# Optimization experiments

Measured on AMD Instinct MI355X. Metric: run time of the kernel, lower is better.

The kernel has to match this reference:

```python
import jax, jax.numpy as jnp
from jax import lax
import numpy as np

B = 33  # block size hard-coded in the original model
BB = B * B  # 1089


def _blockify(img):
    # img: [S, H*33, L*33] -> [1089, L*H*S], column order (l major, h, s)
    S = img.shape[0]; H = img.shape[1] // B; L = img.shape[2] // B
    x = img.reshape(S, H, B, L, B).transpose(3, 1, 0, 2, 4)  # [L,H,S,33,33]
    return x.reshape(L * H * S, BB).T


def _unblockify(X, S, H, L):
    # X: [1089, L*H*S] -> [S, H*33, L*33]
    x = X.T.reshape(L, H, S, B, B).transpose(2, 1, 3, 0, 4)  # [S,H,33,L,33]
    return x.reshape(S, H * B, L * B)


def _conv(x, w):
    return lax.conv_general_dilated(x, w, (1, 1), 'SAME',
                                    dimension_numbers=('NCHW', 'OIHW', 'NCHW'))


def _cnn(x, w1, b1, w2, b2, w3, b3, w4):
    # 4-layer CNN used by both Denoiser and Deblocker; x: [N,1,h,w]
    x = jax.nn.relu(_conv(x, w1) + b1[None, :, None, None])
    x = jax.nn.relu(_conv(x, w2) + b2[None, :, None, None])
    x = jax.nn.relu(_conv(x, w3) + b3[None, :, None, None])
    return _conv(x, w4)  # final conv has no bias


def _denoise(X, w1, b1, w2, b2, w3, b3, w4):
    # X: [1089, N] -> per-block CNN -> [1089, N]
    N = X.shape[1]
    x = X.T.reshape(N, 1, B, B)
    out = _cnn(x, w1, b1, w2, b2, w3, b3, w4)
    return out[:, 0].reshape(N, BB).T


def _deblock(img, w1, b1, w2, b2, w3, b3, w4):
    # img: [S, Hp, Wp] -> [S, Hp, Wp]
    return _cnn(img[:, None], w1, b1, w2, b2, w3, b3, w4)[:, 0]


def setup_inputs() -> dict:
    key = jax.random.key(0)
    ks = jax.random.split(key, 20)
    S, H, L, M, layers = 8, 8, 8, 272, 5
    wstd = 0.05
    def w(k, shape):
        return jax.random.normal(k, shape, jnp.float32) * wstd
    inp = {}
    inp['inputs'] = jax.random.normal(ks[0], (S, 1, H * B, L * B), jnp.float32)
    A = jax.random.normal(ks[1], (M, BB), jnp.float32) / np.float32(np.sqrt(BB))
    inp['A'] = A
    inp['Q'] = A.T
    inp['steps'] = jnp.ones((layers,), jnp.float32)
    inp['den_w1'] = w(ks[2], (layers, 32, 1, 3, 3))
    inp['den_b1'] = jnp.zeros((layers, 32), jnp.float32)
    inp['den_w2'] = w(ks[3], (layers, 32, 32, 3, 3))
    inp['den_b2'] = jnp.zeros((layers, 32), jnp.float32)
    inp['den_w3'] = w(ks[4], (layers, 32, 32, 3, 3))
    inp['den_b3'] = jnp.zeros((layers, 32), jnp.float32)
    inp['den_w4'] = w(ks[5], (layers, 1, 32, 3, 3))
    inp['deb_w1'] = w(ks[6], (layers, 32, 1, 3, 3))
    inp['deb_b1'] = jnp.zeros((layers, 32), jnp.float32)
    inp['deb_w2'] = w(ks[7], (layers, 32, 32, 3, 3))
    inp['deb_b2'] = jnp.zeros((layers, 32), jnp.float32)
    inp['deb_w3'] = w(ks[8], (layers, 32, 32, 3, 3))
    inp['deb_b3'] = jnp.zeros((layers, 32), jnp.float32)
    inp['deb_w4'] = w(ks[9], (layers, 1, 32, 3, 3))
    inp['output_layers'] = layers
    return inp


def reference(inputs, A, Q, steps,
              den_w1, den_b1, den_w2, den_b2, den_w3, den_b3, den_w4,
              deb_w1, deb_b1, deb_w2, deb_b2, deb_w3, deb_b3, deb_w4,
              output_layers):
    S = inputs.shape[0]
    H = inputs.shape[2] // B
    L = inputs.shape[3] // B
    Xb = _blockify(inputs[:, 0])          # [1089, N]
    y = A @ Xb                             # sampling: [M, N]
    X = Q @ y                              # initial reconstruction [1089, N]
    I = jnp.eye(BB, dtype=A.dtype)
    AtA = A.T @ A                          # original recomputes each layer; same math
    for n in range(output_layers):
        step = steps[n]
        z = step * (A.T @ (y - A @ X)) + X
        noise = _denoise(X, den_w1[n], den_b1[n], den_w2[n], den_b2[n],
                         den_w3[n], den_b3[n], den_w4[n])
        X = z - (step * AtA - I) @ noise
        img = _unblockify(X, S, H, L)
        img = img - _deblock(img, deb_w1[n], deb_b1[n], deb_w2[n], deb_b2[n],
                             deb_w3[n], deb_b3[n], deb_w4[n])
        X = _blockify(img)
    return _unblockify(X, S, H, L)[:, None]  # [S,1,H*33,L*33]
```

## Files before the change

### kernel.cpp

```cpp
#include <hip/hip_runtime.h>
#include <hip/hip_fp16.h>

#define BLKSZ 33
#define NBB   1089
#define IMW   264

typedef _Float16 f16x8 __attribute__((ext_vector_type(8)));
typedef float f32x4 __attribute__((ext_vector_type(4)));

__global__ __launch_bounds__(256) void blockify_k(const float* __restrict__ in,
                                                  float* __restrict__ X, int S) {
  int gid = blockIdx.x * 256 + threadIdx.x;
  int total = S * 64 * NBB;
  if (gid >= total) return;
  int n = gid / NBB, p = gid - n * NBB;
  int l = n >> 6, h = (n >> 3) & 7, s = n & 7;
  int i = p / BLKSZ, j = p - i * BLKSZ;
  X[gid] = in[((size_t)s * IMW + h * BLKSZ + i) * IMW + l * BLKSZ + j];
}

__global__ __launch_bounds__(256) void gemm_nt_sk(
    const float* __restrict__ Am, const float* __restrict__ Bm,
    float* __restrict__ P, int M, int N, int K, int lda, int ldb, int SK) {
  __shared__ float As[16][68];
  __shared__ float Bs[16][68];
  int tid = threadIdx.x;
  int tx = tid & 15, ty = tid >> 4;
  int bi = blockIdx.y * 64, bj = blockIdx.x * 64;
  int sk = blockIdx.z;
  int chunk = (((K + SK - 1) / SK) + 15) & ~15;
  int kbeg = sk * chunk;
  int kend = kbeg + chunk; if (kend > K) kend = K;
  float acc[4][4] = {{0.f, 0.f, 0.f, 0.f}, {0.f, 0.f, 0.f, 0.f},
                     {0.f, 0.f, 0.f, 0.f}, {0.f, 0.f, 0.f, 0.f}};
  float ra[4], rb[4];
  {
    int kk = kbeg + tx;
#pragma unroll
    for (int t = 0; t < 4; ++t) {
      int r = ty + t * 16;
      ra[t] = (bi + r < M && kk < kend) ? Am[(size_t)(bi + r) * lda + kk] : 0.f;
      rb[t] = (bj + r < N && kk < kend) ? Bm[(size_t)(bj + r) * ldb + kk] : 0.f;
    }
  }
  for (int k0 = kbeg; k0 < kend; k0 += 16) {
#pragma unroll
    for (int t = 0; t < 4; ++t) {
      int r = ty + t * 16;
      As[tx][r] = ra[t];
      Bs[tx][r] = rb[t];
    }
    __syncthreads();
    if (k0 + 16 < kend) {
      int kk = k0 + 16 + tx;
#pragma unroll
      for (int t = 0; t < 4; ++t) {
        int r = ty + t * 16;
        ra[t] = (bi + r < M && kk < kend) ? Am[(size_t)(bi + r) * lda + kk] : 0.f;
        rb[t] = (bj + r < N && kk < kend) ? Bm[(size_t)(bj + r) * ldb + kk] : 0.f;
      }
    }
#pragma unroll
    for (int kk = 0; kk < 16; ++kk) {
      float4 av = *(const float4*)&As[kk][ty * 4];
      float4 bv = *(const float4*)&Bs[kk][tx * 4];
      acc[0][0] += av.x * bv.x; acc[0][1] += av.x * bv.y; acc[0][2] += av.x * bv.z; acc[0][3] += av.x * bv.w;
      acc[1][0] += av.y * bv.x; acc[1][1] += av.y * bv.y; acc[1][2] += av.y * bv.z; acc[1][3] += av.y * bv.w;
      acc[2][0] += av.z * bv.x; acc[2][1] += av.z * bv.y; acc[2][2] += av.z * bv.z; acc[2][3] += av.z * bv.w;
      acc[3][0] += av.w * bv.x; acc[3][1] += av.w * bv.y; acc[3][2] += av.w * bv.z; acc[3][3] += av.w * bv.w;
    }
    __syncthreads();
  }
  size_t base = (size_t)sk * M * N;
#pragma unroll
  for (int r = 0; r < 4; ++r) {
    int i = bi + ty * 4 + r;
    if (i >= M) continue;
#pragma unroll
    for (int c = 0; c < 4; ++c) {
      int j = bj + tx * 4 + c;
      if (j < N) P[base + (size_t)i * N + j] = acc[r][c];
    }
  }
}

__global__ __launch_bounds__(256) void reduce_sk_k(
    const float* __restrict__ P, float* __restrict__ C, float* __restrict__ C2,
    long long total, long long stride, int SK, int mode,
    const float* __restrict__ step_ptr, const float* __restrict__ src1,
    const float* __restrict__ src2) {
  long long gid = (long long)blockIdx.x * 256 + threadIdx.x;
  if (gid >= total) return;
  float s = 0.f;
  for (int k = 0; k < SK; ++k) s += P[(size_t)k * stride + gid];
  if (mode == 0) {
    C[gid] = s;
    if (C2) C2[gid] = s;
  } else {
    float st = step_ptr[0];
    float v = src1[gid] - st * s + st * src2[gid];
    int n = (int)(gid / NBB), p = (int)(gid - (long long)n * NBB);
    int l = n >> 6, h = (n >> 3) & 7, s_ = n & 7;
    int i = p / BLKSZ, j = p - i * BLKSZ;
    C[((size_t)s_ * IMW + h * BLKSZ + i) * IMW + l * BLKSZ + j] = v;
  }
}

__global__ __launch_bounds__(256) void pack_w_k(const float* __restrict__ w0,
                                                const float* __restrict__ w1,
                                                const float* __restrict__ w2,
                                                const float* __restrict__ w3,
                                                __half* __restrict__ wp, int layers) {
  int gid = blockIdx.x * 256 + threadIdx.x;
  int total = layers * 4 * 9216;
  if (gid >= total) return;
  int slot = gid / 9216, r = gid - slot * 9216;
  int n = slot >> 2, which = slot & 3;
  int tap = r / 1024, r2 = r - tap * 1024;
  int co = r2 >> 5, ci = r2 & 31;
  const float* src = (which == 0) ? w0 : (which == 1) ? w1 : (which == 2) ? w2 : w3;
  wp[gid] = __float2half(src[n * 9216 + (co * 32 + ci) * 9 + tap]);
}

__global__ __launch_bounds__(256) void zero_borders1_k(__half* __restrict__ a,
                                                       int nimg, int H, int W) {
  int Wp = W + 2, Hp = H + 2;
  int perim = 2 * Wp + 2 * H;
  int gid = blockIdx.x * 256 + threadIdx.x;
  int total = nimg * perim;
  if (gid >= total) return;
  int img = gid / perim, k = gid - img * perim;
  int row, col;
  if (k < Wp)            { row = 0;      col = k; }
  else if (k < 2 * Wp)   { row = Hp - 1; col = k - Wp; }
  else { int k2 = k - 2 * Wp; row = 1 + (k2 >> 1); col = (k2 & 1) ? (Wp - 1) : 0; }
  size_t off = ((size_t)(img * Hp + row) * Wp + col) * 32;
  float4 z = {0.f, 0.f, 0.f, 0.f};
  float4* pa = (float4*)(a + off);
#pragma unroll
  for (int q = 0; q < 4; ++q) pa[q] = z;
}

__global__ __launch_bounds__(256) void conv1_k(const float* __restrict__ in,
                                               __half* __restrict__ out,
                                               const float* __restrict__ w,
                                               const float* __restrict__ b,
                                               int nimg, int H, int W) {
  __shared__ float wl[9][32];
  __shared__ float bl[32];
  int tid = threadIdx.x;
  for (int t = tid; t < 288; t += 256) {
    int co = t / 9, tap = t - co * 9;
    wl[tap][co] = w[t];
  }
  if (tid < 32) bl[tid] = b[tid];
  __syncthreads();
  int Hp = H + 2, Wp = W + 2;
  int gid = blockIdx.x * 256 + tid;
  if (gid >= nimg * Hp * Wp) return;
  int img = gid / (Hp * Wp);
  int rem = gid - img * (Hp * Wp);
  int yy = rem / Wp, xx = rem - yy * Wp;
  size_t ob = ((size_t)(img * Hp + yy) * Wp + xx) * 32;
  if (yy == 0 || yy == Hp - 1 || xx == 0 || xx == Wp - 1) {
    float4 z = {0.f, 0.f, 0.f, 0.f};
#pragma unroll
    for (int q = 0; q < 4; ++q) *(float4*)(out + ob + 8 * q) = z;
    return;
  }
  int y = yy - 1, x = xx - 1;
  float acc[32];
#pragma unroll
  for (int c = 0; c < 32; ++c) acc[c] = bl[c];
  const float* ip = in + (size_t)img * H * W;
#pragma unroll
  for (int ty = 0; ty < 3; ++ty)
#pragma unroll
    for (int tx = 0; tx < 3; ++tx) {
      int yv = y + ty - 1, xv = x + tx - 1;
      if (yv >= 0 && yv < H && xv >= 0 && xv < W) {
        float v = ip[(size_t)yv * W + xv];
        const float* wp = &wl[ty * 3 + tx][0];
#pragma unroll
        for (int q = 0; q < 8; ++q) {
          float4 wv = *(const float4*)(wp + q * 4);
          acc[q * 4 + 0] += v * wv.x; acc[q * 4 + 1] += v * wv.y;
          acc[q * 4 + 2] += v * wv.z; acc[q * 4 + 3] += v * wv.w;
        }
      }
    }
  __half2* op = (__half2*)(out + ob);
#pragma unroll
  for (int c2 = 0; c2 < 16; ++c2)
    op[c2] = __floats2half2_rn(fmaxf(acc[2 * c2], 0.f), fmaxf(acc[2 * c2 + 1], 0.f));
}

__global__ __launch_bounds__(256) void conv2_mfma_k(const __half* __restrict__ in,
                                                    __half* __restrict__ out,
                                                    const __half* __restrict__ wp,
                                                    const float* __restrict__ bias,
                                                    int nimg, int H, int W, int CH) {
  int ntx = (W + 15) >> 4;
  int nch = (H + CH - 1) / CH;
  int wid = blockIdx.x * 4 + (threadIdx.x >> 6);
  int total = nimg * 2 * ntx * nch;
  if (wid >= total) return;
  int lane = threadIdx.x & 63;
  int m16 = lane & 15, kg = lane >> 4;
  int yc = wid % nch; int t = wid / nch;
  int xt = t % ntx; t /= ntx;
  int cohalf = t & 1; int img = t >> 1;
  int Wp = W + 2, Hp = H + 2, Hpm1 = Hp - 1;
  const __half* wq = wp + (cohalf * 16 + m16) * 32 + kg * 8;
  f16x8 bfr0 = *(const f16x8*)(wq + 0 * 1024);
  f16x8 bfr1 = *(const f16x8*)(wq + 1 * 1024);
  f16x8 bfr2 = *(const f16x8*)(wq + 2 * 1024);
  f16x8 bfr3 = *(const f16x8*)(wq + 3 * 1024);
  f16x8 bfr4 = *(const f16x8*)(wq + 4 * 1024);
  f16x8 bfr5 = *(const f16x8*)(wq + 5 * 1024);
  f16x8 bfr6 = *(const f16x8*)(wq + 6 * 1024);
  f16x8 bfr7 = *(const f16x8*)(wq + 7 * 1024);
  f16x8 bfr8 = *(const f16x8*)(wq + 8 * 1024);
  float bv = bias[cohalf * 16 + m16];
  int x0 = xt << 4;
  int y1 = yc * CH + 1;
  int y2 = y1 + CH - 1; if (y2 > H) y2 = H;
  int c0 = x0 + m16;     if (c0 > W + 1) c0 = W + 1; c0 *= 32;
  int c1 = x0 + m16 + 1; if (c1 > W + 1) c1 = W + 1; c1 *= 32;
  int c2 = x0 + m16 + 2; if (c2 > W + 1) c2 = W + 1; c2 *= 32;
  size_t ibase = (size_t)img * Hp;
  int cohalf16 = cohalf * 16;

#define LOADROW(row, d0, d1, d2) { int rr = (row); if (rr > Hpm1) rr = Hpm1;    \
    const __half* rp = in + (ibase + rr) * (size_t)Wp * 32 + kg * 8;            \
    d0 = *(const f16x8*)(rp + c0); d1 = *(const f16x8*)(rp + c1);               \
    d2 = *(const f16x8*)(rp + c2); }

#define CITER(yo, A0_,A1_,A2_, B0_,B1_,B2_, C0_,C1_,C2_, P0_,P1_,P2_) {         \
    LOADROW((yo) + 3, P0_, P1_, P2_);                                           \
    f32x4 a0 = {0.f, 0.f, 0.f, 0.f}, a1 = {0.f, 0.f, 0.f, 0.f};                 \
    a0 = __builtin_amdgcn_mfma_f32_16x16x32_f16(A0_, bfr0, a0, 0, 0, 0);        \
    a1 = __builtin_amdgcn_mfma_f32_16x16x32_f16(A1_, bfr1, a1, 0, 0, 0);        \
    a0 = __builtin_amdgcn_mfma_f32_16x16x32_f16(A2_, bfr2, a0, 0, 0, 0);        \
    a1 = __builtin_amdgcn_mfma_f32_16x16x32_f16(B0_, bfr3, a1, 0, 0, 0);        \
    a0 = __builtin_amdgcn_mfma_f32_16x16x32_f16(B1_, bfr4, a0, 0, 0, 0);        \
    a1 = __builtin_amdgcn_mfma_f32_16x16x32_f16(B2_, bfr5, a1, 0, 0, 0);        \
    a0 = __builtin_amdgcn_mfma_f32_16x16x32_f16(C0_, bfr6, a0, 0, 0, 0);        \
    a1 = __builtin_amdgcn_mfma_f32_16x16x32_f16(C1_, bfr7, a1, 0, 0, 0);        \
    a0 = __builtin_amdgcn_mfma_f32_16x16x32_f16(C2_, bfr8, a0, 0, 0, 0);        \
    __half* op = out + (ibase + (yo)) * (size_t)Wp * 32 + cohalf16 + m16;       \
    _Pragma("unroll")                                                           \
    for (int r = 0; r < 4; ++r) { int xo = x0 + kg * 4 + r;                     \
      if (xo < W) op[(xo + 1) * 32] = __float2half(fmaxf(a0[r] + a1[r] + bv, 0.f)); } }

  f16x8 A0,A1,A2,B0,B1,B2,C0,C1,C2,D0,D1,D2,E0,E1,E2;
  LOADROW(y1 - 1, A0, A1, A2);
  LOADROW(y1,     B0, B1, B2);
  LOADROW(y1 + 1, C0, C1, C2);
  LOADROW(y1 + 2, D0, D1, D2);
  int yo = y1;
  for (; yo + 4 <= y2; yo += 5) {
    CITER(yo,     A0,A1,A2, B0,B1,B2, C0,C1,C2, E0,E1,E2);
    CITER(yo + 1, B0,B1,B2, C0,C1,C2, D0,D1,D2, A0,A1,A2);
    CITER(yo + 2, C0,C1,C2, D0,D1,D2, E0,E1,E2, B0,B1,B2);
    CITER(yo + 3, D0,D1,D2, E0,E1,E2, A0,A1,A2, C0,C1,C2);
    CITER(yo + 4, E0,E1,E2, A0,A1,A2, B0,B1,B2, D0,D1,D2);
  }
  if (yo <= y2) { CITER(yo, A0,A1,A2, B0,B1,B2, C0,C1,C2, E0,E1,E2); ++yo; }
  if (yo <= y2) { CITER(yo, B0,B1,B2, C0,C1,C2, D0,D1,D2, A0,A1,A2); ++yo; }
  if (yo <= y2) { CITER(yo, C0,C1,C2, D0,D1,D2, E0,E1,E2, B0,B1,B2); ++yo; }
  if (yo <= y2) { CITER(yo, D0,D1,D2, E0,E1,E2, A0,A1,A2, C0,C1,C2); ++yo; }
#undef CITER
#undef LOADROW
}

__global__ __launch_bounds__(256) void conv4_k(const __half* __restrict__ in,
                                               float* __restrict__ out,
                                               const float* __restrict__ w,
                                               const float* __restrict__ src,
                                               int nimg, int H, int W, float sign, int perm) {
  __shared__ float wl[9][32];
  int tid = threadIdx.x;
  for (int t = tid; t < 288; t += 256) {
    int ci = t / 9, tap = t - ci * 9;
    wl[tap][ci] = w[t];
  }
  __syncthreads();
  int gid = blockIdx.x * 256 + tid;
  if (gid >= nimg * H * W) return;
  int img = gid / (H * W);
  int rem = gid - img * H * W;
  int y = rem / W, x = rem - y * W;
  int Wp = W + 2;
  float acc = 0.f;
#pragma unroll
  for (int ty = 0; ty < 3; ++ty)
#pragma unroll
    for (int tx = 0; tx < 3; ++tx) {
      const f16x8* ip = (const f16x8*)(in + ((size_t)(img * (H + 2) + y + ty) * Wp + x + tx) * 32);
      const float* wpt = &wl[ty * 3 + tx][0];
#pragma unroll
      for (int q = 0; q < 4; ++q) {
        f16x8 v = ip[q];
#pragma unroll
        for (int e = 0; e < 8; ++e) acc += (float)v[e] * wpt[q * 8 + e];
      }
    }
  float val = src[gid] + sign * acc;
  if (perm) {
    int h = y / BLKSZ, i = y - h * BLKSZ;
    int l = x / BLKSZ, j = x - l * BLKSZ;
    out[(size_t)(l * 64 + h * 8 + img) * NBB + i * BLKSZ + j] = val;
  } else {
    out[gid] = val;
  }
}

__global__ __launch_bounds__(256) void denoise_fused_k(
    const float* __restrict__ X, float* __restrict__ T,
    const float* __restrict__ w1, const float* __restrict__ b1,
    const __half* __restrict__ wp2, const float* __restrict__ b2,
    const __half* __restrict__ wp3, const float* __restrict__ b3,
    const float* __restrict__ w4) {
  __shared__ __align__(16) __half Abuf[35 * 35 * 32];
  __shared__ __align__(16) __half Bbuf[35 * 35 * 32];
  __shared__ float wl1[9][32];
  __shared__ float wl4[9][32];
  __shared__ float bl1[32];
  int tid = threadIdx.x;
  int img = blockIdx.x;
  int wave = tid >> 6, lane = tid & 63;
  int m16 = lane & 15, kg = lane >> 4;

  for (int t = tid; t < 288; t += 256) {
    int c = t / 9, tap = t - c * 9;
    wl1[tap][c] = w1[t];
    wl4[tap][c] = w4[t];
  }
  if (tid < 32) bl1[tid] = b1[tid];
  float* Xs = (float*)Bbuf;
  const float* Xg = X + (size_t)img * NBB;
  for (int t = tid; t < NBB; t += 256) Xs[t] = Xg[t];
  __syncthreads();

  for (int cell = tid; cell < 1225; cell += 256) {
    int yy = cell / 35, xx = cell - yy * 35;
    __half* oc = Abuf + cell * 32;
    if (yy == 0 || yy == 34 || xx == 0 || xx == 34) {
      f16x8 hz = {};
#pragma unroll
      for (int q = 0; q < 4; ++q) *(f16x8*)(oc + 8 * q) = hz;
      continue;
    }
    int y = yy - 1, x = xx - 1;
    float acc[32];
#pragma unroll
    for (int c = 0; c < 32; ++c) acc[c] = bl1[c];
#pragma unroll
    for (int dy = 0; dy < 3; ++dy)
#pragma unroll
      for (int dx = 0; dx < 3; ++dx) {
        int yv = y + dy - 1, xv = x + dx - 1;
        if (yv >= 0 && yv < 33 && xv >= 0 && xv < 33) {
          float v = Xs[yv * 33 + xv];
          const float* wp = &wl1[dy * 3 + dx][0];
#pragma unroll
          for (int q = 0; q < 8; ++q) {
            float4 wv = *(const float4*)(wp + q * 4);
            acc[q * 4 + 0] += v * wv.x; acc[q * 4 + 1] += v * wv.y;
            acc[q * 4 + 2] += v * wv.z; acc[q * 4 + 3] += v * wv.w;
          }
        }
      }
    __half2* op = (__half2*)oc;
#pragma unroll
    for (int c2 = 0; c2 < 16; ++c2)
      op[c2] = __floats2half2_rn(fmaxf(acc[2 * c2], 0.f), fmaxf(acc[2 * c2 + 1], 0.f));
  }
  __syncthreads();

#define CONV2LDS(SRC, DST, WPTR, BPTR) {                                        \
  _Pragma("unroll 1")                                                           \
  for (int jid = wave; jid < 12; jid += 4) {                                    \
    int cohalf = jid & 1;                                                       \
    int xt = (jid >> 1) % 3;                                                    \
    int yh = jid / 6;                                                           \
    const __half* wq = WPTR + (cohalf * 16 + m16) * 32 + kg * 8;                \
    f16x8 bfr0 = *(const f16x8*)(wq + 0 * 1024);                                \
    f16x8 bfr1 = *(const f16x8*)(wq + 1 * 1024);                                \
    f16x8 bfr2 = *(const f16x8*)(wq + 2 * 1024);                                \
    f16x8 bfr3 = *(const f16x8*)(wq + 3 * 1024);                                \
    f16x8 bfr4 = *(const f16x8*)(wq + 4 * 1024);                                \
    f16x8 bfr5 = *(const f16x8*)(wq + 5 * 1024);                                \
    f16x8 bfr6 = *(const f16x8*)(wq + 6 * 1024);                                \
    f16x8 bfr7 = *(const f16x8*)(wq + 7 * 1024);                                \
    f16x8 bfr8 = *(const f16x8*)(wq + 8 * 1024);                                \
    float bv = BPTR[cohalf * 16 + m16];                                         \
    int x0 = xt << 4;                                                           \
    int y1 = 1 + yh * 17;                                                       \
    int y2 = yh ? 33 : 17;                                                      \
    int c0 = x0 + m16;     if (c0 > 34) c0 = 34; c0 *= 32;                      \
    int c1 = x0 + m16 + 1; if (c1 > 34) c1 = 34; c1 *= 32;                      \
    int c2 = x0 + m16 + 2; if (c2 > 34) c2 = 34; c2 *= 32;                      \
    int cohalf16 = cohalf * 16;                                                 \
    f16x8 A0,A1,A2,B0,B1,B2,C0,C1,C2,D0,D1,D2,E0,E1,E2;                         \
    LROW(SRC, y1 - 1, A0, A1, A2);                                              \
    LROW(SRC, y1,     B0, B1, B2);                                              \
    LROW(SRC, y1 + 1, C0, C1, C2);                                              \
    LROW(SRC, y1 + 2, D0, D1, D2);                                              \
    int yo = y1;                                                                \
    for (; yo + 4 <= y2; yo += 5) {                                             \
      CIT(SRC, DST, yo,     A0,A1,A2, B0,B1,B2, C0,C1,C2, E0,E1,E2);            \
      CIT(SRC, DST, yo + 1, B0,B1,B2, C0,C1,C2, D0,D1,D2, A0,A1,A2);            \
      CIT(SRC, DST, yo + 2, C0,C1,C2, D0,D1,D2, E0,E1,E2, B0,B1,B2);            \
      CIT(SRC, DST, yo + 3, D0,D1,D2, E0,E1,E2, A0,A1,A2, C0,C1,C2);            \
      CIT(SRC, DST, yo + 4, E0,E1,E2, A0,A1,A2, B0,B1,B2, D0,D1,D2);            \
    }                                                                           \
    if (yo <= y2) { CIT(SRC, DST, yo, A0,A1,A2, B0,B1,B2, C0,C1,C2, E0,E1,E2); ++yo; } \
    if (yo <= y2) { CIT(SRC, DST, yo, B0,B1,B2, C0,C1,C2, D0,D1,D2, A0,A1,A2); ++yo; } \
    if (yo <= y2) { CIT(SRC, DST, yo, C0,C1,C2, D0,D1,D2, E0,E1,E2, B0,B1,B2); ++yo; } \
    if (yo <= y2) { CIT(SRC, DST, yo, D0,D1,D2, E0,E1,E2, A0,A1,A2, C0,C1,C2); ++yo; } \
  } }

#define LROW(SRC, row, d0, d1, d2) { int rr = (row); if (rr > 34) rr = 34;      \
    const __half* rp = SRC + rr * 35 * 32 + kg * 8;                             \
    d0 = *(const f16x8*)(rp + c0); d1 = *(const f16x8*)(rp + c1);               \
    d2 = *(const f16x8*)(rp + c2); }

#define CIT(SRC, DST, yo, A0_,A1_,A2_, B0_,B1_,B2_, C0_,C1_,C2_, P0_,P1_,P2_) { \
    LROW(SRC, (yo) + 3, P0_, P1_, P2_);                                         \
    f32x4 a0 = {0.f, 0.f, 0.f, 0.f}, a1 = {0.f, 0.f, 0.f, 0.f};                 \
    a0 = __builtin_amdgcn_mfma_f32_16x16x32_f16(A0_, bfr0, a0, 0, 0, 0);        \
    a1 = __builtin_amdgcn_mfma_f32_16x16x32_f16(A1_, bfr1, a1, 0, 0, 0);        \
    a0 = __builtin_amdgcn_mfma_f32_16x16x32_f16(A2_, bfr2, a0, 0, 0, 0);        \
    a1 = __builtin_amdgcn_mfma_f32_16x16x32_f16(B0_, bfr3, a1, 0, 0, 0);        \
    a0 = __builtin_amdgcn_mfma_f32_16x16x32_f16(B1_, bfr4, a0, 0, 0, 0);        \
    a1 = __builtin_amdgcn_mfma_f32_16x16x32_f16(B2_, bfr5, a1, 0, 0, 0);        \
    a0 = __builtin_amdgcn_mfma_f32_16x16x32_f16(C0_, bfr6, a0, 0, 0, 0);        \
    a1 = __builtin_amdgcn_mfma_f32_16x16x32_f16(C1_, bfr7, a1, 0, 0, 0);        \
    a0 = __builtin_amdgcn_mfma_f32_16x16x32_f16(C2_, bfr8, a0, 0, 0, 0);        \
    _Pragma("unroll")                                                           \
    for (int r = 0; r < 4; ++r) { int xo = x0 + kg * 4 + r;                     \
      if (xo < 33) DST[(yo) * 35 * 32 + (xo + 1) * 32 + cohalf16 + m16] =       \
        __float2half(fmaxf(a0[r] + a1[r] + bv, 0.f)); } }

  {
    f16x8 hz = {};
    for (int t = tid; t < 544; t += 256) {
      int ci = t >> 2, q = t & 3;
      int cell;
      if (ci < 35)       cell = ci;
      else if (ci < 70)  cell = 34 * 35 + (ci - 35);
      else if (ci < 103) cell = (ci - 70 + 1) * 35;
      else               cell = (ci - 103 + 1) * 35 + 34;
      *(f16x8*)(Bbuf + cell * 32 + q * 8) = hz;
    }
  }
  CONV2LDS(Abuf, Bbuf, wp2, b2);
  __syncthreads();

  CONV2LDS(Bbuf, Abuf, wp3, b3);
  __syncthreads();
#undef CIT
#undef LROW
#undef CONV2LDS

  float* Tg = T + (size_t)img * NBB;
  for (int p = tid; p < NBB; p += 256) {
    int y = p / 33, x = p - y * 33;
    float acc = 0.f;
#pragma unroll
    for (int dy = 0; dy < 3; ++dy)
#pragma unroll
      for (int dx = 0; dx < 3; ++dx) {
        const f16x8* ip = (const f16x8*)(Abuf + ((y + dy) * 35 + x + dx) * 32);
        const float* wpt = &wl4[dy * 3 + dx][0];
#pragma unroll
        for (int q = 0; q < 4; ++q) {
          f16x8 v = ip[q];
#pragma unroll
          for (int e = 0; e < 8; ++e) acc += (float)v[e] * wpt[q * 8 + e];
        }
      }
    Tg[p] = Xg[p] + acc;
  }
}

static inline int cdiv(int a, int b) { return (a + b - 1) / b; }

extern "C" void kernel_launch(void* const* d_in, const int* in_sizes, int n_in,
                              void* d_out, int out_size, void* d_ws, size_t ws_size,
                              hipStream_t stream) {
  const float* d_inputs = (const float*)d_in[0];
  const float* d_A      = (const float*)d_in[1];
  const float* d_Q      = (const float*)d_in[2];
  const float* d_steps  = (const float*)d_in[3];
  const float* den_w1 = (const float*)d_in[4];
  const float* den_b1 = (const float*)d_in[5];
  const float* den_b2 = (const float*)d_in[7];
  const float* den_b3 = (const float*)d_in[9];
  const float* den_w4 = (const float*)d_in[10];
  const float* deb_w1 = (const float*)d_in[11];
  const float* deb_b1 = (const float*)d_in[12];
  const float* deb_b2 = (const float*)d_in[14];
  const float* deb_b3 = (const float*)d_in[16];
  const float* deb_w4 = (const float*)d_in[17];

  int layers = in_sizes[3];
  int M      = in_sizes[1] / NBB;
  int S      = in_sizes[0] / (IMW * IMW);
  int N      = 64 * S;

  float* ws    = (float*)d_ws;
  float* AtA   = ws;
  float* X     = AtA + 1185936;
  float* T     = X + (size_t)N * NBB;
  float* X0    = T + (size_t)N * NBB;
  float* y2    = X0 + (size_t)N * NBB;
  float* img   = y2 + (size_t)N * M;
  float* Pbuf  = img + (size_t)S * IMW * IMW;
  __half* wph  = (__half*)(Pbuf + (size_t)8 * N * NBB);
  __half* buf1 = wph + (size_t)layers * 4 * 9216 + 2048;
  size_t bufElems = (size_t)S * 266 * 266 * 32;
  __half* buf2 = buf1 + bufElems;

  dim3 blk(256);

  pack_w_k<<<cdiv(layers * 4 * 9216, 256), blk, 0, stream>>>(
      (const float*)d_in[6], (const float*)d_in[8], (const float*)d_in[13],
      (const float*)d_in[15], wph, layers);
  blockify_k<<<cdiv(N * NBB, 256), blk, 0, stream>>>(d_inputs, T, S);

  gemm_nt_sk<<<dim3(cdiv(NBB, 64), cdiv(NBB, 64), 2), blk, 0, stream>>>(
      d_Q, d_Q, Pbuf, NBB, NBB, M, M, M, 2);
  reduce_sk_k<<<cdiv(NBB * NBB, 256), blk, 0, stream>>>(
      Pbuf, AtA, nullptr, (long long)NBB * NBB, (long long)NBB * NBB, 2, 0,
      nullptr, nullptr, nullptr);
  gemm_nt_sk<<<dim3(cdiv(M, 64), cdiv(N, 64), 8), blk, 0, stream>>>(
      T, d_A, Pbuf, N, M, NBB, NBB, NBB, 8);
  reduce_sk_k<<<cdiv(N * M, 256), blk, 0, stream>>>(
      Pbuf, y2, nullptr, (long long)N * M, (long long)N * M, 8, 0,
      nullptr, nullptr, nullptr);
  gemm_nt_sk<<<dim3(cdiv(NBB, 64), cdiv(N, 64), 4), blk, 0, stream>>>(
      y2, d_Q, Pbuf, N, NBB, M, M, M, 4);
  reduce_sk_k<<<cdiv(N * NBB, 256), blk, 0, stream>>>(
      Pbuf, X0, X, (long long)N * NBB, (long long)N * NBB, 4, 0,
      nullptr, nullptr, nullptr);

  const int CH_DEB = 12;
  int deb_waves = S * 2 * cdiv(IMW, 16) * cdiv(IMW, CH_DEB);

  for (int n = 0; n < layers; ++n) {
    const float* stepp = d_steps + n;

    denoise_fused_k<<<N, blk, 0, stream>>>(
        X, T, den_w1 + n * 288, den_b1 + n * 32,
        wph + (size_t)(n * 4 + 0) * 9216, den_b2 + n * 32,
        wph + (size_t)(n * 4 + 1) * 9216, den_b3 + n * 32,
        den_w4 + n * 288);

    gemm_nt_sk<<<dim3(cdiv(NBB, 64), cdiv(N, 64), 8), blk, 0, stream>>>(
        T, AtA, Pbuf, N, NBB, NBB, NBB, NBB, 8);
    reduce_sk_k<<<cdiv(N * NBB, 256), blk, 0, stream>>>(
        Pbuf, img, nullptr, (long long)N * NBB, (long long)N * NBB, 8, 4,
        stepp, T, X0);

    zero_borders1_k<<<cdiv(S * (2 * 266 + 2 * 264), 256), blk, 0, stream>>>(
        buf2, S, IMW, IMW);
    conv1_k<<<cdiv(S * 266 * 266, 256), blk, 0, stream>>>(
        img, buf1, deb_w1 + n * 288, deb_b1 + n * 32, S, IMW, IMW);
    conv2_mfma_k<<<cdiv(deb_waves, 4), blk, 0, stream>>>(
        buf1, buf2, wph + (size_t)(n * 4 + 2) * 9216, deb_b2 + n * 32, S, IMW, IMW, CH_DEB);
    conv2_mfma_k<<<cdiv(deb_waves, 4), blk, 0, stream>>>(
        buf2, buf1, wph + (size_t)(n * 4 + 3) * 9216, deb_b3 + n * 32, S, IMW, IMW, CH_DEB);
    if (n < layers - 1) {
      conv4_k<<<cdiv(S * IMW * IMW, 256), blk, 0, stream>>>(
          buf1, X, deb_w4 + n * 288, img, S, IMW, IMW, -1.f, 1);
    } else {
      conv4_k<<<cdiv(S * IMW * IMW, 256), blk, 0, stream>>>(
          buf1, (float*)d_out, deb_w4 + n * 288, img, S, IMW, IMW, -1.f, 0);
    }
  }
}
```

Baseline: 1.288 ms.

## Compute both output-channel halves per wave, use fdot2 in final conv, widen denoiser block

In the deblocker's MFMA conv, each wave now produces all 32 output channels, so every loaded input row feeds both channel halves and input loads are halved, at the cost of holding twice the weight fragments in registers. The final 32-to-1 convolutions (conv4_k and the denoiser tail) keep their weights as packed fp16 pairs and use the fdot2 builtin instead of scalar fp32 multiply-adds, which adds fp16 rounding of the weights. The fused denoiser kernel moves from 256 to 512 threads, splits the conv work into 24 smaller row jobs, and adds a barrier after border zeroing.

```diff
diff --git a/kernel.cpp b/kernel.cpp
--- a/kernel.cpp
+++ b/kernel.cpp
@@ -6,7 +6,16 @@
 #define IMW   264
 
 typedef _Float16 f16x8 __attribute__((ext_vector_type(8)));
+typedef _Float16 f16x2 __attribute__((ext_vector_type(2)));
 typedef float f32x4 __attribute__((ext_vector_type(4)));
+
+__device__ __forceinline__ float dot2f(f16x2 a, f16x2 b, float c) {
+#if __has_builtin(__builtin_amdgcn_fdot2)
+  return __builtin_amdgcn_fdot2(a, b, c, false);
+#else
+  return c + (float)a[0] * (float)b[0] + (float)a[1] * (float)b[1];
+#endif
+}
 
 __global__ __launch_bounds__(256) void blockify_k(const float* __restrict__ in,
                                                   float* __restrict__ X, int S) {
@@ -203,25 +212,25 @@
   int ntx = (W + 15) >> 4;
   int nch = (H + CH - 1) / CH;
   int wid = blockIdx.x * 4 + (threadIdx.x >> 6);
-  int total = nimg * 2 * ntx * nch;
+  int total = nimg * ntx * nch;
   if (wid >= total) return;
   int lane = threadIdx.x & 63;
   int m16 = lane & 15, kg = lane >> 4;
   int yc = wid % nch; int t = wid / nch;
-  int xt = t % ntx; t /= ntx;
-  int cohalf = t & 1; int img = t >> 1;
+  int xt = t % ntx; int img = t / ntx;
   int Wp = W + 2, Hp = H + 2, Hpm1 = Hp - 1;
-  const __half* wq = wp + (cohalf * 16 + m16) * 32 + kg * 8;
-  f16x8 bfr0 = *(const f16x8*)(wq + 0 * 1024);
-  f16x8 bfr1 = *(const f16x8*)(wq + 1 * 1024);
-  f16x8 bfr2 = *(const f16x8*)(wq + 2 * 1024);
-  f16x8 bfr3 = *(const f16x8*)(wq + 3 * 1024);
-  f16x8 bfr4 = *(const f16x8*)(wq + 4 * 1024);
-  f16x8 bfr5 = *(const f16x8*)(wq + 5 * 1024);
-  f16x8 bfr6 = *(const f16x8*)(wq + 6 * 1024);
-  f16x8 bfr7 = *(const f16x8*)(wq + 7 * 1024);
-  f16x8 bfr8 = *(const f16x8*)(wq + 8 * 1024);
-  float bv = bias[cohalf * 16 + m16];
+  const __half* wqA = wp + m16 * 32 + kg * 8;
+  const __half* wqB = wp + (16 + m16) * 32 + kg * 8;
+  f16x8 bA0 = *(const f16x8*)(wqA + 0 * 1024), bB0 = *(const f16x8*)(wqB + 0 * 1024);
+  f16x8 bA1 = *(const f16x8*)(wqA + 1 * 1024), bB1 = *(const f16x8*)(wqB + 1 * 1024);
+  f16x8 bA2 = *(const f16x8*)(wqA + 2 * 1024), bB2 = *(const f16x8*)(wqB + 2 * 1024);
+  f16x8 bA3 = *(const f16x8*)(wqA + 3 * 1024), bB3 = *(const f16x8*)(wqB + 3 * 1024);
+  f16x8 bA4 = *(const f16x8*)(wqA + 4 * 1024), bB4 = *(const f16x8*)(wqB + 4 * 1024);
+  f16x8 bA5 = *(const f16x8*)(wqA + 5 * 1024), bB5 = *(const f16x8*)(wqB + 5 * 1024);
+  f16x8 bA6 = *(const f16x8*)(wqA + 6 * 1024), bB6 = *(const f16x8*)(wqB + 6 * 1024);
+  f16x8 bA7 = *(const f16x8*)(wqA + 7 * 1024), bB7 = *(const f16x8*)(wqB + 7 * 1024);
+  f16x8 bA8 = *(const f16x8*)(wqA + 8 * 1024), bB8 = *(const f16x8*)(wqB + 8 * 1024);
+  float bvA = bias[m16], bvB = bias[16 + m16];
   int x0 = xt << 4;
   int y1 = yc * CH + 1;
   int y2 = y1 + CH - 1; if (y2 > H) y2 = H;
@@ -229,7 +238,6 @@
   int c1 = x0 + m16 + 1; if (c1 > W + 1) c1 = W + 1; c1 *= 32;
   int c2 = x0 + m16 + 2; if (c2 > W + 1) c2 = W + 1; c2 *= 32;
   size_t ibase = (size_t)img * Hp;
-  int cohalf16 = cohalf * 16;
 
 #define LOADROW(row, d0, d1, d2) { int rr = (row); if (rr > Hpm1) rr = Hpm1;    \
     const __half* rp = in + (ibase + rr) * (size_t)Wp * 32 + kg * 8;            \
@@ -238,20 +246,32 @@
 
 #define CITER(yo, A0_,A1_,A2_, B0_,B1_,B2_, C0_,C1_,C2_, P0_,P1_,P2_) {         \
     LOADROW((yo) + 3, P0_, P1_, P2_);                                           \
-    f32x4 a0 = {0.f, 0.f, 0.f, 0.f}, a1 = {0.f, 0.f, 0.f, 0.f};                 \
-    a0 = __builtin_amdgcn_mfma_f32_16x16x32_f16(A0_, bfr0, a0, 0, 0, 0);        \
-    a1 = __builtin_amdgcn_mfma_f32_16x16x32_f16(A1_, bfr1, a1, 0, 0, 0);        \
-    a0 = __builtin_amdgcn_mfma_f32_16x16x32_f16(A2_, bfr2, a0, 0, 0, 0);        \
-    a1 = __builtin_amdgcn_mfma_f32_16x16x32_f16(B0_, bfr3, a1, 0, 0, 0);        \
-    a0 = __builtin_amdgcn_mfma_f32_16x16x32_f16(B1_, bfr4, a0, 0, 0, 0);        \
-    a1 = __builtin_amdgcn_mfma_f32_16x16x32_f16(B2_, bfr5, a1, 0, 0, 0);        \
-    a0 = __builtin_amdgcn_mfma_f32_16x16x32_f16(C0_, bfr6, a0, 0, 0, 0);        \
-    a1 = __builtin_amdgcn_mfma_f32_16x16x32_f16(C1_, bfr7, a1, 0, 0, 0);        \
-    a0 = __builtin_amdgcn_mfma_f32_16x16x32_f16(C2_, bfr8, a0, 0, 0, 0);        \
-    __half* op = out + (ibase + (yo)) * (size_t)Wp * 32 + cohalf16 + m16;       \
+    f32x4 aA0 = {0.f,0.f,0.f,0.f}, aA1 = {0.f,0.f,0.f,0.f};                     \
+    f32x4 aB0 = {0.f,0.f,0.f,0.f}, aB1 = {0.f,0.f,0.f,0.f};                     \
+    aA0 = __builtin_amdgcn_mfma_f32_16x16x32_f16(A0_, bA0, aA0, 0, 0, 0);       \
+    aB0 = __builtin_amdgcn_mfma_f32_16x16x32_f16(A0_, bB0, aB0, 0, 0, 0);       \
+    aA1 = __builtin_amdgcn_mfma_f32_16x16x32_f16(A1_, bA1, aA1, 0, 0, 0);       \
+    aB1 = __builtin_amdgcn_mfma_f32_16x16x32_f16(A1_, bB1, aB1, 0, 0, 0);       \
+    aA0 = __builtin_amdgcn_mfma_f32_16x16x32_f16(A2_, bA2, aA0, 0, 0, 0);       \
+    aB0 = __builtin_amdgcn_mfma_f32_16x16x32_f16(A2_, bB2, aB0, 0, 0, 0);       \
+    aA1 = __builtin_amdgcn_mfma_f32_16x16x32_f16(B0_, bA3, aA1, 0, 0, 0);       \
+    aB1 = __builtin_amdgcn_mfma_f32_16x16x32_f16(B0_, bB3, aB1, 0, 0, 0);       \
+    aA0 = __builtin_amdgcn_mfma_f32_16x16x32_f16(B1_, bA4, aA0, 0, 0, 0);       \
+    aB0 = __builtin_amdgcn_mfma_f32_16x16x32_f16(B1_, bB4, aB0, 0, 0, 0);       \
+    aA1 = __builtin_amdgcn_mfma_f32_16x16x32_f16(B2_, bA5, aA1, 0, 0, 0);       \
+    aB1 = __builtin_amdgcn_mfma_f32_16x16x32_f16(B2_, bB5, aB1, 0, 0, 0);       \
+    aA0 = __builtin_amdgcn_mfma_f32_16x16x32_f16(C0_, bA6, aA0, 0, 0, 0);       \
+    aB0 = __builtin_amdgcn_mfma_f32_16x16x32_f16(C0_, bB6, aB0, 0, 0, 0);       \
+    aA1 = __builtin_amdgcn_mfma_f32_16x16x32_f16(C1_, bA7, aA1, 0, 0, 0);       \
+    aB1 = __builtin_amdgcn_mfma_f32_16x16x32_f16(C1_, bB7, aB1, 0, 0, 0);       \
+    aA0 = __builtin_amdgcn_mfma_f32_16x16x32_f16(C2_, bA8, aA0, 0, 0, 0);       \
+    aB0 = __builtin_amdgcn_mfma_f32_16x16x32_f16(C2_, bB8, aB0, 0, 0, 0);       \
+    __half* op = out + (ibase + (yo)) * (size_t)Wp * 32;                        \
     _Pragma("unroll")                                                           \
     for (int r = 0; r < 4; ++r) { int xo = x0 + kg * 4 + r;                     \
-      if (xo < W) op[(xo + 1) * 32] = __float2half(fmaxf(a0[r] + a1[r] + bv, 0.f)); } }
+      if (xo < W) { __half* o2 = op + (xo + 1) * 32;                            \
+        o2[m16]      = __float2half(fmaxf(aA0[r] + aA1[r] + bvA, 0.f));         \
+        o2[16 + m16] = __float2half(fmaxf(aB0[r] + aB1[r] + bvB, 0.f)); } } }
 
   f16x8 A0,A1,A2,B0,B1,B2,C0,C1,C2,D0,D1,D2,E0,E1,E2;
   LOADROW(y1 - 1, A0, A1, A2);
@@ -279,11 +299,14 @@
                                                const float* __restrict__ w,
                                                const float* __restrict__ src,
                                                int nimg, int H, int W, float sign, int perm) {
-  __shared__ float wl[9][32];
+  __shared__ f16x2 wl[9][16];
   int tid = threadIdx.x;
-  for (int t = tid; t < 288; t += 256) {
-    int ci = t / 9, tap = t - ci * 9;
-    wl[tap][ci] = w[t];
+  for (int t = tid; t < 144; t += 256) {
+    int tap = t % 9, c2 = t / 9;
+    f16x2 h;
+    h[0] = (_Float16)w[(2 * c2) * 9 + tap];
+    h[1] = (_Float16)w[(2 * c2 + 1) * 9 + tap];
+    wl[tap][c2] = h;
   }
   __syncthreads();
   int gid = blockIdx.x * 256 + tid;
@@ -298,12 +321,13 @@
 #pragma unroll
     for (int tx = 0; tx < 3; ++tx) {
       const f16x8* ip = (const f16x8*)(in + ((size_t)(img * (H + 2) + y + ty) * Wp + x + tx) * 32);
-      const float* wpt = &wl[ty * 3 + tx][0];
+      const f16x2* wpt = &wl[ty * 3 + tx][0];
 #pragma unroll
       for (int q = 0; q < 4; ++q) {
         f16x8 v = ip[q];
-#pragma unroll
-        for (int e = 0; e < 8; ++e) acc += (float)v[e] * wpt[q * 8 + e];
+        const f16x2* pv = (const f16x2*)&v;
+#pragma unroll
+        for (int e = 0; e < 4; ++e) acc = dot2f(pv[e], wpt[q * 4 + e], acc);
       }
     }
   float val = src[gid] + sign * acc;
@@ -316,7 +340,7 @@
   }
 }
 
-__global__ __launch_bounds__(256) void denoise_fused_k(
+__global__ __launch_bounds__(512) void denoise_fused_k(
     const float* __restrict__ X, float* __restrict__ T,
     const float* __restrict__ w1, const float* __restrict__ b1,
     const __half* __restrict__ wp2, const float* __restrict__ b2,
@@ -325,25 +349,31 @@
   __shared__ __align__(16) __half Abuf[35 * 35 * 32];
   __shared__ __align__(16) __half Bbuf[35 * 35 * 32];
   __shared__ float wl1[9][32];
-  __shared__ float wl4[9][32];
+  __shared__ f16x2 wl4h[9][16];
   __shared__ float bl1[32];
   int tid = threadIdx.x;
   int img = blockIdx.x;
   int wave = tid >> 6, lane = tid & 63;
   int m16 = lane & 15, kg = lane >> 4;
 
-  for (int t = tid; t < 288; t += 256) {
+  for (int t = tid; t < 288; t += 512) {
     int c = t / 9, tap = t - c * 9;
     wl1[tap][c] = w1[t];
-    wl4[tap][c] = w4[t];
+  }
+  for (int t = tid; t < 144; t += 512) {
+    int tap = t % 9, c2 = t / 9;
+    f16x2 h;
+    h[0] = (_Float16)w4[(2 * c2) * 9 + tap];
+    h[1] = (_Float16)w4[(2 * c2 + 1) * 9 + tap];
+    wl4h[tap][c2] = h;
   }
   if (tid < 32) bl1[tid] = b1[tid];
   float* Xs = (float*)Bbuf;
   const float* Xg = X + (size_t)img * NBB;
-  for (int t = tid; t < NBB; t += 256) Xs[t] = Xg[t];
+  for (int t = tid; t < NBB; t += 512) Xs[t] = Xg[t];
   __syncthreads();
 
-  for (int cell = tid; cell < 1225; cell += 256) {
+  for (int cell = tid; cell < 1225; cell += 512) {
     int yy = cell / 35, xx = cell - yy * 35;
     __half* oc = Abuf + cell * 32;
     if (yy == 0 || yy == 34 || xx == 0 || xx == 34) {
@@ -381,7 +411,7 @@
 
 #define CONV2LDS(SRC, DST, WPTR, BPTR) {                                        \
   _Pragma("unroll 1")                                                           \
-  for (int jid = wave; jid < 12; jid += 4) {                                    \
+  for (int jid = wave; jid < 24; jid += 8) {                                    \
     int cohalf = jid & 1;                                                       \
     int xt = (jid >> 1) % 3;                                                    \
     int yh = jid / 6;                                                           \
@@ -397,8 +427,8 @@
     f16x8 bfr8 = *(const f16x8*)(wq + 8 * 1024);                                \
     float bv = BPTR[cohalf * 16 + m16];                                         \
     int x0 = xt << 4;                                                           \
-    int y1 = 1 + yh * 17;                                                       \
-    int y2 = yh ? 33 : 17;                                                      \
+    int y1 = 1 + yh * 9;                                                        \
+    int y2 = y1 + 8; if (y2 > 33) y2 = 33;                                      \
     int c0 = x0 + m16;     if (c0 > 34) c0 = 34; c0 *= 32;                      \
     int c1 = x0 + m16 + 1; if (c1 > 34) c1 = 34; c1 *= 32;                      \
     int c2 = x0 + m16 + 2; if (c2 > 34) c2 = 34; c2 *= 32;                      \
@@ -446,7 +476,7 @@
 
   {
     f16x8 hz = {};
-    for (int t = tid; t < 544; t += 256) {
+    for (int t = tid; t < 544; t += 512) {
       int ci = t >> 2, q = t & 3;
       int cell;
       if (ci < 35)       cell = ci;
@@ -456,6 +486,7 @@
       *(f16x8*)(Bbuf + cell * 32 + q * 8) = hz;
     }
   }
+  __syncthreads();
   CONV2LDS(Abuf, Bbuf, wp2, b2);
   __syncthreads();
 
@@ -466,7 +497,7 @@
 #undef CONV2LDS
 
   float* Tg = T + (size_t)img * NBB;
-  for (int p = tid; p < NBB; p += 256) {
+  for (int p = tid; p < NBB; p += 512) {
     int y = p / 33, x = p - y * 33;
     float acc = 0.f;
 #pragma unroll
@@ -474,12 +505,13 @@
 #pragma unroll
       for (int dx = 0; dx < 3; ++dx) {
         const f16x8* ip = (const f16x8*)(Abuf + ((y + dy) * 35 + x + dx) * 32);
-        const float* wpt = &wl4[dy * 3 + dx][0];
+        const f16x2* wpt = &wl4h[dy * 3 + dx][0];
 #pragma unroll
         for (int q = 0; q < 4; ++q) {
           f16x8 v = ip[q];
-#pragma unroll
-          for (int e = 0; e < 8; ++e) acc += (float)v[e] * wpt[q * 8 + e];
+          const f16x2* pv = (const f16x2*)&v;
+#pragma unroll
+          for (int e = 0; e < 4; ++e) acc = dot2f(pv[e], wpt[q * 4 + e], acc);
         }
       }
     Tg[p] = Xg[p] + acc;
@@ -548,12 +580,12 @@
       nullptr, nullptr, nullptr);
 
   const int CH_DEB = 12;
-  int deb_waves = S * 2 * cdiv(IMW, 16) * cdiv(IMW, CH_DEB);
+  int deb_jobs = S * cdiv(IMW, 16) * cdiv(IMW, CH_DEB);
 
   for (int n = 0; n < layers; ++n) {
     const float* stepp = d_steps + n;
 
-    denoise_fused_k<<<N, blk, 0, stream>>>(
+    denoise_fused_k<<<N, dim3(512), 0, stream>>>(
         X, T, den_w1 + n * 288, den_b1 + n * 32,
         wph + (size_t)(n * 4 + 0) * 9216, den_b2 + n * 32,
         wph + (size_t)(n * 4 + 1) * 9216, den_b3 + n * 32,
@@ -569,9 +601,9 @@
         buf2, S, IMW, IMW);
     conv1_k<<<cdiv(S * 266 * 266, 256), blk, 0, stream>>>(
         img, buf1, deb_w1 + n * 288, deb_b1 + n * 32, S, IMW, IMW);
-    conv2_mfma_k<<<cdiv(deb_waves, 4), blk, 0, stream>>>(
+    conv2_mfma_k<<<cdiv(deb_jobs, 4), blk, 0, stream>>>(
         buf1, buf2, wph + (size_t)(n * 4 + 2) * 9216, deb_b2 + n * 32, S, IMW, IMW, CH_DEB);
-    conv2_mfma_k<<<cdiv(deb_waves, 4), blk, 0, stream>>>(
+    conv2_mfma_k<<<cdiv(deb_jobs, 4), blk, 0, stream>>>(
         buf2, buf1, wph + (size_t)(n * 4 + 3) * 9216, deb_b3 + n * 32, S, IMW, IMW, CH_DEB);
     if (n < layers - 1) {
       conv4_k<<<cdiv(S * IMW * IMW, 256), blk, 0, stream>>>(
```

After: 1.381 ms. 1.07x slower.
